# Optimization experiments

Hardware: AMD Instinct MI355X
Metric: run time of the kernel (lower is better)

Reference implementation:

```python
import jax, jax.numpy as jnp
import numpy as np

NT, NRV, NR = 100000, 200000, 300000  # tile / road_vertex / road node counts
E = 400000                             # edges per edge type
B, H, P, A = 64, 128, 64, 512          # graphs, hidden, player_state_dim, action_dim


def _gat(h_src, h_dst, src, dst, W, a_s, a_d, b, n_dst):
    # PyG GATConv, heads=1, shared lin for src/dst, no self loops (bipartite)
    hs = h_src @ W                      # [Ns, H]
    hd = h_dst @ W                      # [Nd, H]
    e = jax.nn.leaky_relu((hs @ a_s)[src] + (hd @ a_d)[dst], 0.2)  # [E]
    m = jax.ops.segment_max(e, dst, num_segments=n_dst)
    w = jnp.exp(e - m[dst])
    denom = jax.ops.segment_sum(w, dst, num_segments=n_dst)
    alpha = w / jnp.maximum(denom[dst], 1e-16)                      # segment softmax
    out = jax.ops.segment_sum(alpha[:, None] * hs[src], dst, num_segments=n_dst)
    return out + b


def _mean_pool(x, batch, nb):
    s = jax.ops.segment_sum(x, batch, num_segments=nb)
    c = jax.ops.segment_sum(jnp.ones((x.shape[0],), x.dtype), batch, num_segments=nb)
    return s / jnp.maximum(c, 1.0)[:, None]


def setup_inputs():
    ks = iter(jax.random.split(jax.random.key(0), 64))
    f32 = jnp.float32

    def lin(i, o):
        return (jax.random.normal(next(ks), (i, o), f32) / np.float32(np.sqrt(i)))

    d = {}
    d['x_tile'] = jax.random.normal(next(ks), (NT, 8), f32)
    d['x_rv'] = jax.random.normal(next(ks), (NRV, 13), f32)
    d['x_road'] = jax.random.normal(next(ks), (NR, 4), f32)
    d['x_player'] = jax.random.normal(next(ks), (B, P), f32)
    # node encoders
    d['enc_t_W'] = lin(8, H);  d['enc_t_b'] = jnp.zeros((H,), f32)
    d['enc_rv_W'] = lin(13, H); d['enc_rv_b'] = jnp.zeros((H,), f32)
    d['enc_r_W'] = lin(4, H);  d['enc_r_b'] = jnp.zeros((H,), f32)
    # six GAT convs
    for name in ['rv2t', 't2rv', 'r2rv', 'rv2r', 't2r', 'r2t']:
        d[name + '_W'] = lin(H, H)
        d[name + '_as'] = jax.random.normal(next(ks), (H,), f32) * 0.1
        d[name + '_ad'] = jax.random.normal(next(ks), (H,), f32) * 0.1
        d[name + '_b'] = jnp.zeros((H,), f32)
    # player MLP + output head (input: 3H pooled + H player)
    d['fc1_W'] = lin(P, H); d['fc1_b'] = jnp.zeros((H,), f32)
    d['fc2_W'] = lin(H, H); d['fc2_b'] = jnp.zeros((H,), f32)
    d['out_W'] = lin(4 * H, A); d['out_b'] = jnp.zeros((A,), f32)
    # edges (src bounded by source-type count, dst by dest-type count)
    ri = lambda n, hi: jax.random.randint(n, (E,), 0, hi, jnp.int32)
    d['e_rv2t_src'] = ri(next(ks), NRV); d['e_rv2t_dst'] = ri(next(ks), NT)
    d['e_t2rv_src'] = ri(next(ks), NT);  d['e_t2rv_dst'] = ri(next(ks), NRV)
    d['e_r2rv_src'] = ri(next(ks), NR);  d['e_r2rv_dst'] = ri(next(ks), NRV)
    d['e_rv2r_src'] = ri(next(ks), NRV); d['e_rv2r_dst'] = ri(next(ks), NR)
    d['e_t2r_src'] = ri(next(ks), NT);   d['e_t2r_dst'] = ri(next(ks), NR)
    d['e_r2t_src'] = ri(next(ks), NR);   d['e_r2t_dst'] = ri(next(ks), NT)
    # batch assignment per node type
    d['batch_tile'] = jnp.sort(jax.random.randint(next(ks), (NT,), 0, B, jnp.int32))
    d['batch_rv'] = jnp.sort(jax.random.randint(next(ks), (NRV,), 0, B, jnp.int32))
    d['batch_road'] = jnp.sort(jax.random.randint(next(ks), (NR,), 0, B, jnp.int32))
    return d


def reference(x_tile, x_rv, x_road, x_player,
              enc_t_W, enc_t_b, enc_rv_W, enc_rv_b, enc_r_W, enc_r_b,
              rv2t_W, rv2t_as, rv2t_ad, rv2t_b,
              t2rv_W, t2rv_as, t2rv_ad, t2rv_b,
              r2rv_W, r2rv_as, r2rv_ad, r2rv_b,
              rv2r_W, rv2r_as, rv2r_ad, rv2r_b,
              t2r_W, t2r_as, t2r_ad, t2r_b,
              r2t_W, r2t_as, r2t_ad, r2t_b,
              fc1_W, fc1_b, fc2_W, fc2_b, out_W, out_b,
              e_rv2t_src, e_rv2t_dst, e_t2rv_src, e_t2rv_dst,
              e_r2rv_src, e_r2rv_dst, e_rv2r_src, e_rv2r_dst,
              e_t2r_src, e_t2r_dst, e_r2t_src, e_r2t_dst,
              batch_tile, batch_rv, batch_road):
    # node encoders
    h_t = x_tile @ enc_t_W + enc_t_b
    h_rv = x_rv @ enc_rv_W + enc_rv_b
    h_r = x_road @ enc_r_W + enc_r_b
    # hetero GAT, aggr='sum' over edge types per destination node type
    o_t = (_gat(h_rv, h_t, e_rv2t_src, e_rv2t_dst, rv2t_W, rv2t_as, rv2t_ad, rv2t_b, NT)
           + _gat(h_r, h_t, e_r2t_src, e_r2t_dst, r2t_W, r2t_as, r2t_ad, r2t_b, NT))
    o_rv = (_gat(h_t, h_rv, e_t2rv_src, e_t2rv_dst, t2rv_W, t2rv_as, t2rv_ad, t2rv_b, NRV)
            + _gat(h_r, h_rv, e_r2rv_src, e_r2rv_dst, r2rv_W, r2rv_as, r2rv_ad, r2rv_b, NRV))
    o_r = (_gat(h_rv, h_r, e_rv2r_src, e_rv2r_dst, rv2r_W, rv2r_as, rv2r_ad, rv2r_b, NR)
           + _gat(h_t, h_r, e_t2r_src, e_t2r_dst, t2r_W, t2r_as, t2r_ad, t2r_b, NR))
    # global mean pool per node type, concat -> [B, 3H]
    x_all = jnp.concatenate([_mean_pool(o_t, batch_tile, B),
                             _mean_pool(o_rv, batch_rv, B),
                             _mean_pool(o_r, batch_road, B)], axis=1)
    # player branch
    p = jax.nn.relu(x_player @ fc1_W + fc1_b)
    p = jax.nn.relu(p @ fc2_W + fc2_b)
    x = jnp.concatenate([x_all, p], axis=1)  # [B, 4H]
    return x @ out_W + out_b                 # [B, A]
```

## Files before the change

kernel.cpp:

```cpp
#include <hip/hip_runtime.h>


constexpr int kNT = 100000, kNRV = 200000, kNR = 300000, kE = 400000;
constexpr int kEq   = kE / 4;
constexpr int kSLOT = 1088;
constexpr int kNBB  = 1024;

typedef _Float16 h2v __attribute__((ext_vector_type(2)));

constexpr long long OFF_C    = 0;
constexpr long long OFF_VS   = 13056;
constexpr long long OFF_VD   = 13176;
constexpr long long OFF_BD   = 13296;
constexpr long long OFF_PS   = 13512;
constexpr long long OFF_XCAT = 22216;
constexpr long long OFF_LS16 = 54984;
constexpr long long OFF_LD16 = 654984;
constexpr long long OFF_PB   = 54984;
constexpr long long OFF_W16  = 1254984;
constexpr long long OFF_DN   = 2454984;
constexpr long long OFF_XR   = 3654984;

__constant__ const int kLSB[6]  = {0, 200000, 300000, 600000, 800000, 900000};
__constant__ const int kDRB[6]  = {0, 100000, 300000, 500000, 800000, 1100000};
__constant__ const int kDLEN[6] = {100000, 200000, 200000, 300000, 300000, 100000};
__constant__ const int kDstT[6] = {0, 1, 1, 2, 2, 0};
__constant__ const int cSlotEt[8]  = {1, 2, 4, 5, 0, 0, 3, 3};
__constant__ const int cSlotLo[8]  = {0, 0, 0, 0, 0, 100000, 0, 100000};
__constant__ const int cSlotHi[8]  = {1 << 30, 1 << 30, 1 << 30, 1 << 30,
                                      100000, 200000, 100000, 200000};
__constant__ const int cSlotCnt[8] = {1, 1, 1, 1, 1, 0, 1, 0};

__device__ __forceinline__ int lowb(const int* a, int n, int v) {
  int lo = 0, hi = n;
  while (lo < hi) { int mid = (lo + hi) >> 1; if (a[mid] < v) lo = mid + 1; else hi = mid; }
  return lo;
}

__global__ __launch_bounds__(256) void precompute_kernel(
    const float* encW_t, const float* encb_t,
    const float* encW_rv, const float* encb_rv,
    const float* encW_r, const float* encb_r,
    const float* W0, const float* as0, const float* ad0,
    const float* W1, const float* as1, const float* ad1,
    const float* W2, const float* as2, const float* ad2,
    const float* W3, const float* as3, const float* ad3,
    const float* W4, const float* as4, const float* ad4,
    const float* W5, const float* as5, const float* ad5,
    const int* bt, const int* brv, const int* br,
    float* Cws, float* vsw, float* vdw, int* BD)
{
  int tid = threadIdx.x;
  if (blockIdx.x == 24) {
    if (tid < 3 * 65) {
      int tt = tid / 65, q = tid - tt * 65;
      const int* ba = (tt == 0) ? bt : (tt == 1 ? brv : br);
      int N = (tt == 0) ? kNT : (tt == 1 ? kNRV : kNR);
      BD[tt * 72 + q] = lowb(ba, N, q);
    }
    return;
  }
  const float* encW[3] = {encW_t, encW_rv, encW_r};
  const float* encb[3] = {encb_t, encb_rv, encb_r};
  const int    Ks[3]   = {8, 13, 4};
  const float* Wv[6]  = {W0, W1, W2, W3, W4, W5};
  const float* asv[6] = {as0, as1, as2, as3, as4, as5};
  const float* adv[6] = {ad0, ad1, ad2, ad3, ad4, ad5};
  const int srcT[6] = {1, 0, 2, 1, 0, 2};
  const int dstT[6] = {0, 1, 1, 2, 2, 0};

  int et = blockIdx.x >> 2;
  int jc = blockIdx.x & 3;
  int st = srcT[et], dt = dstT[et];
  const float* eW = encW[st];
  const float* eB = encb[st];
  int K = Ks[st];
  const float* W = Wv[et];

  float* Cslot = Cws + et * 2176;
  for (int idx = tid; idx < (K + 1) * 32; idx += 256) {
    int r = idx >> 5, jj = idx & 31;
    int j = jc * 32 + jj;
    const float* row = (r < K) ? (eW + r * 128) : eB;
    float acc = 0.f;
    for (int m = 0; m < 128; ++m) acc += row[m] * W[m * 128 + j];
    Cslot[(r < K) ? (r * 128 + j) : (2048 + j)] = acc;
  }

  if (jc == 0) {
    __shared__ float us[128], wvs[128];
    const float* a_s = asv[et];
    const float* a_d = adv[et];
    if (tid < 128) {
      float acc = 0.f;
      for (int j = 0; j < 128; ++j) acc += W[tid * 128 + j] * a_s[j];
      us[tid] = acc;
    } else {
      int m = tid - 128;
      float acc = 0.f;
      for (int j = 0; j < 128; ++j) acc += W[m * 128 + j] * a_d[j];
      wvs[m] = acc;
    }
    __syncthreads();
    if (tid <= K) {
      const float* row = (tid < K) ? (eW + tid * 128) : eB;
      float acc = 0.f;
      for (int m = 0; m < 128; ++m) acc += row[m] * us[m];
      vsw[et * 20 + (tid < K ? tid : 16)] = acc;
    }
    int KD = Ks[dt];
    if (tid >= 32 && tid <= 32 + KD) {
      int k = tid - 32;
      const float* row = (k < KD) ? (encW[dt] + k * 128) : encb[dt];
      float acc = 0.f;
      for (int m = 0; m < 128; ++m) acc += row[m] * wvs[m];
      vdw[et * 20 + (k < KD ? k : 16)] = acc;
    }
  }
}

template <int K, int RH>
__device__ __forceinline__ void prep_one(
    const float* __restrict__ xr,
    const float* __restrict__ vsA, const float* __restrict__ vsB,
    const float* __restrict__ vdA, const float* __restrict__ vdB,
    _Float16* lsA, _Float16* lsB, _Float16* ldA, _Float16* ldB,
    float* dnA, float* dnB, _Float16* xrec)
{
  float a0 = 0.f, a1 = 0.f, a2 = 0.f, a3 = 0.f;
#pragma unroll
  for (int k = 0; k < K; ++k) {
    float xv = xr[k];
    a0 += xv * vsA[k]; a1 += xv * vsB[k];
    a2 += xv * vdA[k]; a3 += xv * vdB[k];
    xrec[k] = (_Float16)xv;
  }
#pragma unroll
  for (int k = K; k < RH; ++k) xrec[k] = (_Float16)0.f;
  *lsA = (_Float16)(a0 + vsA[16]);
  *lsB = (_Float16)(a1 + vsB[16]);
  *ldA = (_Float16)(a2 + vdA[16]);
  *ldB = (_Float16)(a3 + vdB[16]);
  *dnA = 0.f;
  *dnB = 0.f;
}

__global__ __launch_bounds__(256) void prep_kernel(
    const float* __restrict__ x_t, const float* __restrict__ x_rv,
    const float* __restrict__ x_r,
    const float* __restrict__ vsw, const float* __restrict__ vdw,
    _Float16* __restrict__ LS16, _Float16* __restrict__ LD16,
    float* __restrict__ DN, _Float16* __restrict__ XR)
{
  int n = blockIdx.x * 256 + threadIdx.x;
  if (n >= kNT + kNRV + kNR) return;
  if (n < kNT) {
    prep_one<8, 8>(x_t + n * 8,
                   vsw + 1 * 20, vsw + 4 * 20, vdw + 0 * 20, vdw + 5 * 20,
                   LS16 + 200000 + n, LS16 + 800000 + n,
                   LD16 + 0 + n, LD16 + 1100000 + n,
                   DN + 0 + n, DN + 1100000 + n,
                   XR + (long long)n * 8);
  } else if (n < kNT + kNRV) {
    int m = n - kNT;
    prep_one<13, 16>(x_rv + m * 13,
                     vsw + 0 * 20, vsw + 3 * 20, vdw + 1 * 20, vdw + 2 * 20,
                     LS16 + 0 + m, LS16 + 600000 + m,
                     LD16 + 100000 + m, LD16 + 300000 + m,
                     DN + 100000 + m, DN + 300000 + m,
                     XR + 800000 + (long long)m * 16);
  } else {
    int m = n - kNT - kNRV;
    prep_one<4, 4>(x_r + m * 4,
                   vsw + 2 * 20, vsw + 5 * 20, vdw + 3 * 20, vdw + 4 * 20,
                   LS16 + 300000 + m, LS16 + 900000 + m,
                   LD16 + 500000 + m, LD16 + 800000 + m,
                   DN + 500000 + m, DN + 800000 + m,
                   XR + 4000000 + (long long)m * 4);
  }
}

__global__ __launch_bounds__(256) void passA_kernel(
    const int* s0, const int* s1, const int* s2,
    const int* s3, const int* s4, const int* s5,
    const int* d0, const int* d1, const int* d2,
    const int* d3, const int* d4, const int* d5,
    const _Float16* __restrict__ LS16, const _Float16* __restrict__ LD16,
    float* __restrict__ DN, _Float16* __restrict__ W16)
{
  int idx = blockIdx.x * 256 + threadIdx.x;
  if (idx >= 6 * kEq) return;
  int et = idx / kEq;
  int q = idx - et * kEq;
  const int* sp; const int* dp;
  switch (et) {
    case 0: sp = s0; dp = d0; break;
    case 1: sp = s1; dp = d1; break;
    case 2: sp = s2; dp = d2; break;
    case 3: sp = s3; dp = d3; break;
    case 4: sp = s4; dp = d4; break;
    default: sp = s5; dp = d5; break;
  }
  int lsb = kLSB[et], drb = kDRB[et];
  int4 ss = ((const int4*)sp)[q];
  int4 dd = ((const int4*)dp)[q];
  int sa[4] = {ss.x, ss.y, ss.z, ss.w};
  int da[4] = {dd.x, dd.y, dd.z, dd.w};
  union { float2 f; _Float16 h[4]; } WU;
  float wa[4];
#pragma unroll
  for (int i = 0; i < 4; ++i) {
    float t = (float)LS16[lsb + sa[i]] + (float)LD16[drb + da[i]];
    t = t > 0.f ? t : 0.2f * t;
    _Float16 h = (_Float16)__expf(t);
    WU.h[i] = h;
    wa[i] = (float)h;
  }
  ((float2*)(W16 + (long long)et * kE))[q] = WU.f;
#pragma unroll
  for (int i = 0; i < 4; ++i) unsafeAtomicAdd(&DN[drb + da[i]], wa[i]);
}

template <int RH>
__device__ __forceinline__ void loadX(const _Float16* __restrict__ xp, float* xv) {
  if constexpr (RH == 4) {
    union { uint2 u; _Float16 h[4]; } U;
    U.u = *(const uint2*)xp;
#pragma unroll
    for (int k = 0; k < RH; ++k) xv[k] = (float)U.h[k];
  } else if constexpr (RH == 8) {
    union { uint4 u; _Float16 h[8]; } U;
    U.u = *(const uint4*)xp;
#pragma unroll
    for (int k = 0; k < RH; ++k) xv[k] = (float)U.h[k];
  } else {
    union { uint4 u[2]; _Float16 h[16]; } U;
    U.u[0] = *(const uint4*)xp;
    U.u[1] = *(const uint4*)(xp + 8);
#pragma unroll
    for (int k = 0; k < RH; ++k) xv[k] = (float)U.h[k];
  }
}

template <int K, int RH>
__device__ __forceinline__ void passB_loop(
    const int* __restrict__ sp, const int* __restrict__ dp,
    const _Float16* __restrict__ Wet, const float* __restrict__ DN, int drb,
    const _Float16* __restrict__ XR, long long xrb,
    const int* __restrict__ bd, float* __restrict__ lp,
    int lo, int hi, int start, int stride)
{
  for (int q = start; q < kEq; q += stride) {
    int4 ss = ((const int4*)sp)[q];
    int4 dd = ((const int4*)dp)[q];
    union { float2 f; _Float16 h[4]; } WU;
    WU.f = ((const float2*)Wet)[q];
    int sa[4] = {ss.x, ss.y, ss.z, ss.w};
    int da[4] = {dd.x, dd.y, dd.z, dd.w};
#pragma unroll
    for (int i = 0; i < 4; ++i) {
      int s = sa[i], d = da[i];
      if (s >= lo && s < hi) {
        float dn = DN[drb + d];
        float alpha = (float)WU.h[i] / fmaxf(dn, 1e-16f);
        int b = 0;
#pragma unroll
        for (int stp = 32; stp >= 1; stp >>= 1) {
          int nb = b + stp;
          if (nb <= 63 && bd[nb] <= d) b = nb;
        }
        float xv[RH];
        loadX<RH>(XR + xrb + (long long)s * RH, xv);
#pragma unroll
        for (int k = 0; k < K; ++k) atomicAdd(lp + k * 64 + b, alpha * xv[k]);
      }
    }
  }
}

__global__ __launch_bounds__(256) void passB_kernel(
    const int* s0, const int* s1, const int* s2,
    const int* s3, const int* s4, const int* s5,
    const int* d0, const int* d1, const int* d2,
    const int* d3, const int* d4, const int* d5,
    const _Float16* __restrict__ W16, const float* __restrict__ DN,
    const _Float16* __restrict__ XR, const int* __restrict__ BDg,
    float* __restrict__ PB)
{
  __shared__ float lp[kSLOT];
  __shared__ int bd[65];
  int tid = threadIdx.x;
  for (int j = tid; j < kSLOT; j += 256) lp[j] = 0.f;
  int slot = blockIdx.x & 7;
  int blk = blockIdx.x >> 3;
  int et = cSlotEt[slot];
  if (tid < 65) bd[tid] = BDg[kDstT[et] * 72 + tid];
  __syncthreads();
  int lo = cSlotLo[slot], hi = cSlotHi[slot];
  int start = blk * 256 + tid;
  int stride = 128 * 256;
  int drb = kDRB[et];
  const _Float16* Wet = W16 + (long long)et * kE;
  switch (et) {
    case 0: passB_loop<13, 16>(s0, d0, Wet, DN, drb, XR, 800000,  bd, lp, lo, hi, start, stride); break;
    case 1: passB_loop< 8,  8>(s1, d1, Wet, DN, drb, XR, 0,       bd, lp, lo, hi, start, stride); break;
    case 2: passB_loop< 4,  4>(s2, d2, Wet, DN, drb, XR, 4000000, bd, lp, lo, hi, start, stride); break;
    case 3: passB_loop<13, 16>(s3, d3, Wet, DN, drb, XR, 800000,  bd, lp, lo, hi, start, stride); break;
    case 4: passB_loop< 8,  8>(s4, d4, Wet, DN, drb, XR, 0,       bd, lp, lo, hi, start, stride); break;
    default: passB_loop<4,  4>(s5, d5, Wet, DN, drb, XR, 4000000, bd, lp, lo, hi, start, stride); break;
  }
  if (cSlotCnt[slot]) {
    int dlen = kDLEN[et];
    for (int j = start; j < dlen; j += stride) {
      if (DN[drb + j] > 0.f) {
        int b = 0;
#pragma unroll
        for (int stp = 32; stp >= 1; stp >>= 1) {
          int nb = b + stp;
          if (nb <= 63 && bd[nb] <= j) b = nb;
        }
        atomicAdd(lp + 1024 + b, 1.f);
      }
    }
  }
  __syncthreads();
  float* dst = PB + (long long)blockIdx.x * kSLOT;
  for (int j = tid; j < kSLOT; j += 256) dst[j] = lp[j];
}

__global__ __launch_bounds__(256) void reduce1_kernel(
    const float* __restrict__ PB, float* __restrict__ PS)
{
  int slot = blockIdx.x / 5;
  int jb = blockIdx.x - slot * 5;
  int j = jb * 256 + threadIdx.x;
  if (j >= kSLOT) return;
  float s = 0.f;
#pragma unroll 8
  for (int blk = 0; blk < 128; ++blk)
    s += PB[(long long)(blk * 8 + slot) * kSLOT + j];
  PS[slot * kSLOT + j] = s;
}

__global__ __launch_bounds__(128) void finalize_kernel(
    const int* __restrict__ BDg,
    const float* __restrict__ xp,
    const float* __restrict__ fc1W, const float* __restrict__ fc1b,
    const float* __restrict__ fc2W, const float* __restrict__ fc2b,
    const float* __restrict__ b_rv2t, const float* __restrict__ b_r2t,
    const float* __restrict__ b_t2rv, const float* __restrict__ b_r2rv,
    const float* __restrict__ b_rv2r, const float* __restrict__ b_t2r,
    const float* __restrict__ Cws, const float* __restrict__ PS,
    float* __restrict__ xcat)
{
  int b = blockIdx.x, tid = threadIdx.x;
  __shared__ float xps[64];
  __shared__ float p1s[128];
  if (tid < 64) xps[tid] = xp[b * 64 + tid];
  __syncthreads();
  float a = fc1b[tid];
  for (int k = 0; k < 64; ++k) a += xps[k] * fc1W[k * 128 + tid];
  p1s[tid] = fmaxf(a, 0.f);
  __syncthreads();
  float a2 = fc2b[tid];
  for (int k = 0; k < 128; ++k) a2 += p1s[k] * fc2W[k * 128 + tid];
  xcat[b * 512 + 384 + tid] = fmaxf(a2, 0.f);

  const int etA[3] = {0, 1, 3}, etB[3] = {5, 2, 4};
  const int KAv[3] = {13, 8, 13}, KBv[3] = {4, 4, 8};
  const int slotA[6] = {4, 0, 1, 6, 2, 3};
  const int slotB[6] = {5, -1, -1, 7, -1, -1};
  for (int t3 = 0; t3 < 3; ++t3) {
    int eA = etA[t3], eB = etB[t3];
    const float* CA = Cws + eA * 2176;
    const float* CB = Cws + eB * 2176;
    int sA1 = slotA[eA], sA2 = slotB[eA];
    int sB1 = slotA[eB], sB2 = slotB[eB];
    const float* PA1 = PS + sA1 * kSLOT;
    const float* PA2 = (sA2 >= 0) ? (PS + sA2 * kSLOT) : nullptr;
    const float* PB1 = PS + sB1 * kSLOT;
    const float* PB2 = (sB2 >= 0) ? (PS + sB2 * kSLOT) : nullptr;
    float cA = PA1[1024 + b] + (PA2 ? PA2[1024 + b] : 0.f);
    float cB = PB1[1024 + b] + (PB2 ? PB2[1024 + b] : 0.f);
    float v = cA * CA[2048 + tid] + cB * CB[2048 + tid];
    for (int k = 0; k < KAv[t3]; ++k) {
      float pv = PA1[k * 64 + b] + (PA2 ? PA2[k * 64 + b] : 0.f);
      v += pv * CA[k * 128 + tid];
    }
    for (int k = 0; k < KBv[t3]; ++k) {
      float pv = PB1[k * 64 + b] + (PB2 ? PB2[k * 64 + b] : 0.f);
      v += pv * CB[k * 128 + tid];
    }
    int cnt = BDg[t3 * 72 + b + 1] - BDg[t3 * 72 + b];
    float cntf = (float)max(cnt, 1);
    const float* bb1 = (t3 == 0) ? b_rv2t : (t3 == 1 ? b_t2rv : b_rv2r);
    const float* bb2 = (t3 == 0) ? b_r2t  : (t3 == 1 ? b_r2rv : b_t2r);
    xcat[b * 512 + t3 * 128 + tid] = v / cntf + bb1[tid] + bb2[tid];
  }
}

__global__ __launch_bounds__(256) void out_kernel(
    const float* __restrict__ xcat, const float* __restrict__ outW,
    const float* __restrict__ outb, float* __restrict__ out)
{
  int g = blockIdx.x * 256 + threadIdx.x;
  int r = g >> 9, c = g & 511;
  const float* xr = xcat + r * 512;
  float acc = outb[c];
  for (int k = 0; k < 512; ++k) acc += xr[k] * outW[k * 512 + c];
  out[g] = acc;
}

extern "C" void kernel_launch(void* const* d_in, const int* in_sizes, int n_in,
                              void* d_out, int out_size, void* d_ws, size_t ws_size,
                              hipStream_t stream) {
  const float* x_tile   = (const float*)d_in[0];
  const float* x_rv     = (const float*)d_in[1];
  const float* x_road   = (const float*)d_in[2];
  const float* x_player = (const float*)d_in[3];
  const float* enc_t_W  = (const float*)d_in[4];
  const float* enc_t_b  = (const float*)d_in[5];
  const float* enc_rv_W = (const float*)d_in[6];
  const float* enc_rv_b = (const float*)d_in[7];
  const float* enc_r_W  = (const float*)d_in[8];
  const float* enc_r_b  = (const float*)d_in[9];
  const float* W[6]; const float* As[6]; const float* Ad[6]; const float* Bb[6];
  for (int et = 0; et < 6; ++et) {
    W[et]  = (const float*)d_in[10 + 4 * et];
    As[et] = (const float*)d_in[11 + 4 * et];
    Ad[et] = (const float*)d_in[12 + 4 * et];
    Bb[et] = (const float*)d_in[13 + 4 * et];
  }
  const float* fc1W = (const float*)d_in[34];
  const float* fc1b = (const float*)d_in[35];
  const float* fc2W = (const float*)d_in[36];
  const float* fc2b = (const float*)d_in[37];
  const float* outW = (const float*)d_in[38];
  const float* outb = (const float*)d_in[39];
  const int* esrc[6]; const int* edst[6];
  for (int et = 0; et < 6; ++et) {
    esrc[et] = (const int*)d_in[40 + 2 * et];
    edst[et] = (const int*)d_in[41 + 2 * et];
  }
  const int* batch_t  = (const int*)d_in[52];
  const int* batch_rv = (const int*)d_in[53];
  const int* batch_r  = (const int*)d_in[54];

  float* wsF = (float*)d_ws;
  float* Cws  = wsF + OFF_C;
  float* vsw  = wsF + OFF_VS;
  float* vdw  = wsF + OFF_VD;
  int*   BD   = (int*)(wsF + OFF_BD);
  float* PS   = wsF + OFF_PS;
  float* xcat = wsF + OFF_XCAT;
  _Float16* LS16 = (_Float16*)(wsF + OFF_LS16);
  _Float16* LD16 = (_Float16*)(wsF + OFF_LD16);
  float* PB   = wsF + OFF_PB;
  _Float16* W16 = (_Float16*)(wsF + OFF_W16);
  float* DN   = wsF + OFF_DN;
  _Float16* XR = (_Float16*)(wsF + OFF_XR);
  float* out  = (float*)d_out;

  precompute_kernel<<<25, 256, 0, stream>>>(
      enc_t_W, enc_t_b, enc_rv_W, enc_rv_b, enc_r_W, enc_r_b,
      W[0], As[0], Ad[0], W[1], As[1], Ad[1], W[2], As[2], Ad[2],
      W[3], As[3], Ad[3], W[4], As[4], Ad[4], W[5], As[5], Ad[5],
      batch_t, batch_rv, batch_r,
      Cws, vsw, vdw, BD);

  prep_kernel<<<(kNT + kNRV + kNR + 255) / 256, 256, 0, stream>>>(
      x_tile, x_rv, x_road, vsw, vdw, LS16, LD16, DN, XR);

  passA_kernel<<<(6 * kEq + 255) / 256, 256, 0, stream>>>(
      esrc[0], esrc[1], esrc[2], esrc[3], esrc[4], esrc[5],
      edst[0], edst[1], edst[2], edst[3], edst[4], edst[5],
      LS16, LD16, DN, W16);

  passB_kernel<<<kNBB, 256, 0, stream>>>(
      esrc[0], esrc[1], esrc[2], esrc[3], esrc[4], esrc[5],
      edst[0], edst[1], edst[2], edst[3], edst[4], edst[5],
      W16, DN, XR, BD, PB);

  reduce1_kernel<<<40, 256, 0, stream>>>(PB, PS);

  finalize_kernel<<<64, 128, 0, stream>>>(
      BD, x_player,
      fc1W, fc1b, fc2W, fc2b,
      Bb[0], Bb[5], Bb[1], Bb[2], Bb[3], Bb[4],
      Cws, PS, xcat);

  out_kernel<<<128, 256, 0, stream>>>(xcat, outW, outb, out);

  (void)in_sizes; (void)n_in; (void)out_size; (void)ws_size;
}
```

Before: 554.1 us.

## Pack reciprocal denominator with graph id into one word; retile passA/passB grids

```diff
diff --git a/kernel.cpp b/kernel.cpp
--- a/kernel.cpp
+++ b/kernel.cpp
@@ -4,9 +4,9 @@
 constexpr int kNT = 100000, kNRV = 200000, kNR = 300000, kE = 400000;
 constexpr int kEq   = kE / 4;
 constexpr int kSLOT = 1088;
-constexpr int kNBB  = 1024;
-
-typedef _Float16 h2v __attribute__((ext_vector_type(2)));
+constexpr int kNBB  = 1536;
+constexpr int kBPS  = 192;
+constexpr int kTOTD = 1200000;
 
 constexpr long long OFF_C    = 0;
 constexpr long long OFF_VS   = 13056;
@@ -16,15 +16,15 @@
 constexpr long long OFF_XCAT = 22216;
 constexpr long long OFF_LS16 = 54984;
 constexpr long long OFF_LD16 = 654984;
-constexpr long long OFF_PB   = 54984;
 constexpr long long OFF_W16  = 1254984;
 constexpr long long OFF_DN   = 2454984;
 constexpr long long OFF_XR   = 3654984;
+constexpr long long OFF_BID  = 6254984;
+constexpr long long OFF_PB   = 6554984;
 
 __constant__ const int kLSB[6]  = {0, 200000, 300000, 600000, 800000, 900000};
 __constant__ const int kDRB[6]  = {0, 100000, 300000, 500000, 800000, 1100000};
 __constant__ const int kDLEN[6] = {100000, 200000, 200000, 300000, 300000, 100000};
-__constant__ const int kDstT[6] = {0, 1, 1, 2, 2, 0};
 __constant__ const int cSlotEt[8]  = {1, 2, 4, 5, 0, 0, 3, 3};
 __constant__ const int cSlotLo[8]  = {0, 0, 0, 0, 0, 100000, 0, 100000};
 __constant__ const int cSlotHi[8]  = {1 << 30, 1 << 30, 1 << 30, 1 << 30,
@@ -121,11 +121,12 @@
 
 template <int K, int RH>
 __device__ __forceinline__ void prep_one(
-    const float* __restrict__ xr,
+    const float* __restrict__ xr, unsigned char b,
     const float* __restrict__ vsA, const float* __restrict__ vsB,
     const float* __restrict__ vdA, const float* __restrict__ vdB,
     _Float16* lsA, _Float16* lsB, _Float16* ldA, _Float16* ldB,
-    float* dnA, float* dnB, _Float16* xrec)
+    float* dnA, float* dnB, unsigned char* bidA, unsigned char* bidB,
+    _Float16* xrec)
 {
   float a0 = 0.f, a1 = 0.f, a2 = 0.f, a3 = 0.f;
 #pragma unroll
@@ -143,39 +144,47 @@
   *ldB = (_Float16)(a3 + vdB[16]);
   *dnA = 0.f;
   *dnB = 0.f;
+  *bidA = b;
+  *bidB = b;
 }
 
 __global__ __launch_bounds__(256) void prep_kernel(
     const float* __restrict__ x_t, const float* __restrict__ x_rv,
     const float* __restrict__ x_r,
+    const int* __restrict__ bt, const int* __restrict__ brv,
+    const int* __restrict__ br,
     const float* __restrict__ vsw, const float* __restrict__ vdw,
     _Float16* __restrict__ LS16, _Float16* __restrict__ LD16,
-    float* __restrict__ DN, _Float16* __restrict__ XR)
+    float* __restrict__ DN, unsigned char* __restrict__ BID,
+    _Float16* __restrict__ XR)
 {
   int n = blockIdx.x * 256 + threadIdx.x;
   if (n >= kNT + kNRV + kNR) return;
   if (n < kNT) {
-    prep_one<8, 8>(x_t + n * 8,
+    prep_one<8, 8>(x_t + n * 8, (unsigned char)bt[n],
                    vsw + 1 * 20, vsw + 4 * 20, vdw + 0 * 20, vdw + 5 * 20,
                    LS16 + 200000 + n, LS16 + 800000 + n,
                    LD16 + 0 + n, LD16 + 1100000 + n,
                    DN + 0 + n, DN + 1100000 + n,
+                   BID + 0 + n, BID + 1100000 + n,
                    XR + (long long)n * 8);
   } else if (n < kNT + kNRV) {
     int m = n - kNT;
-    prep_one<13, 16>(x_rv + m * 13,
+    prep_one<13, 16>(x_rv + m * 13, (unsigned char)brv[m],
                      vsw + 0 * 20, vsw + 3 * 20, vdw + 1 * 20, vdw + 2 * 20,
                      LS16 + 0 + m, LS16 + 600000 + m,
                      LD16 + 100000 + m, LD16 + 300000 + m,
                      DN + 100000 + m, DN + 300000 + m,
+                     BID + 100000 + m, BID + 300000 + m,
                      XR + 800000 + (long long)m * 16);
   } else {
     int m = n - kNT - kNRV;
-    prep_one<4, 4>(x_r + m * 4,
+    prep_one<4, 4>(x_r + m * 4, (unsigned char)br[m],
                    vsw + 2 * 20, vsw + 5 * 20, vdw + 3 * 20, vdw + 4 * 20,
                    LS16 + 300000 + m, LS16 + 900000 + m,
                    LD16 + 500000 + m, LD16 + 800000 + m,
                    DN + 500000 + m, DN + 800000 + m,
+                   BID + 500000 + m, BID + 800000 + m,
                    XR + 4000000 + (long long)m * 4);
   }
 }
@@ -188,37 +197,53 @@
     const _Float16* __restrict__ LS16, const _Float16* __restrict__ LD16,
     float* __restrict__ DN, _Float16* __restrict__ W16)
 {
-  int idx = blockIdx.x * 256 + threadIdx.x;
-  if (idx >= 6 * kEq) return;
-  int et = idx / kEq;
-  int q = idx - et * kEq;
-  const int* sp; const int* dp;
-  switch (et) {
-    case 0: sp = s0; dp = d0; break;
-    case 1: sp = s1; dp = d1; break;
-    case 2: sp = s2; dp = d2; break;
-    case 3: sp = s3; dp = d3; break;
-    case 4: sp = s4; dp = d4; break;
-    default: sp = s5; dp = d5; break;
-  }
-  int lsb = kLSB[et], drb = kDRB[et];
-  int4 ss = ((const int4*)sp)[q];
-  int4 dd = ((const int4*)dp)[q];
-  int sa[4] = {ss.x, ss.y, ss.z, ss.w};
-  int da[4] = {dd.x, dd.y, dd.z, dd.w};
-  union { float2 f; _Float16 h[4]; } WU;
-  float wa[4];
-#pragma unroll
-  for (int i = 0; i < 4; ++i) {
-    float t = (float)LS16[lsb + sa[i]] + (float)LD16[drb + da[i]];
-    t = t > 0.f ? t : 0.2f * t;
-    _Float16 h = (_Float16)__expf(t);
-    WU.h[i] = h;
-    wa[i] = (float)h;
-  }
-  ((float2*)(W16 + (long long)et * kE))[q] = WU.f;
-#pragma unroll
-  for (int i = 0; i < 4; ++i) unsafeAtomicAdd(&DN[drb + da[i]], wa[i]);
+  int slot = blockIdx.x & 7;
+  int blk = blockIdx.x >> 3;
+  for (int i = blk * 256 + (int)threadIdx.x; i < 75000; i += kBPS * 256) {
+    int gq = slot * 75000 + i;
+    int et = gq / 100000;
+    int q = gq - et * 100000;
+    const int* sp; const int* dp;
+    switch (et) {
+      case 0: sp = s0; dp = d0; break;
+      case 1: sp = s1; dp = d1; break;
+      case 2: sp = s2; dp = d2; break;
+      case 3: sp = s3; dp = d3; break;
+      case 4: sp = s4; dp = d4; break;
+      default: sp = s5; dp = d5; break;
+    }
+    int lsb = kLSB[et], drb = kDRB[et];
+    int4 ss = ((const int4*)sp)[q];
+    int4 dd = ((const int4*)dp)[q];
+    int sa[4] = {ss.x, ss.y, ss.z, ss.w};
+    int da[4] = {dd.x, dd.y, dd.z, dd.w};
+    union { float2 f; _Float16 h[4]; } WU;
+    float wa[4];
+#pragma unroll
+    for (int j = 0; j < 4; ++j) {
+      float t = (float)LS16[lsb + sa[j]] + (float)LD16[drb + da[j]];
+      t = t > 0.f ? t : 0.2f * t;
+      _Float16 h = (_Float16)__expf(t);
+      WU.h[j] = h;
+      wa[j] = (float)h;
+    }
+    ((float2*)(W16 + (long long)et * kE))[q] = WU.f;
+#pragma unroll
+    for (int j = 0; j < 4; ++j) unsafeAtomicAdd(&DN[drb + da[j]], wa[j]);
+  }
+}
+
+__global__ __launch_bounds__(256) void pack_kernel(
+    const float* __restrict__ DN, const unsigned char* __restrict__ BID,
+    unsigned* __restrict__ DNu)
+{
+  int j = blockIdx.x * 256 + threadIdx.x;
+  if (j >= kTOTD) return;
+  float dn = DN[j];
+  unsigned u = 0u;
+  if (dn > 0.f)
+    u = (__float_as_uint(1.f / dn) & ~63u) | (unsigned)BID[j];
+  DNu[j] = u;
 }
 
 template <int RH>
@@ -245,10 +270,9 @@
 template <int K, int RH>
 __device__ __forceinline__ void passB_loop(
     const int* __restrict__ sp, const int* __restrict__ dp,
-    const _Float16* __restrict__ Wet, const float* __restrict__ DN, int drb,
+    const _Float16* __restrict__ Wet, const unsigned* __restrict__ DNu, int drb,
     const _Float16* __restrict__ XR, long long xrb,
-    const int* __restrict__ bd, float* __restrict__ lp,
-    int lo, int hi, int start, int stride)
+    float* __restrict__ lp, int lo, int hi, int start, int stride)
 {
   for (int q = start; q < kEq; q += stride) {
     int4 ss = ((const int4*)sp)[q];
@@ -261,14 +285,10 @@
     for (int i = 0; i < 4; ++i) {
       int s = sa[i], d = da[i];
       if (s >= lo && s < hi) {
-        float dn = DN[drb + d];
-        float alpha = (float)WU.h[i] / fmaxf(dn, 1e-16f);
-        int b = 0;
-#pragma unroll
-        for (int stp = 32; stp >= 1; stp >>= 1) {
-          int nb = b + stp;
-          if (nb <= 63 && bd[nb] <= d) b = nb;
-        }
+        unsigned u = DNu[drb + d];
+        int b = (int)(u & 63u);
+        float rinv = __uint_as_float(u & ~63u);
+        float alpha = (float)WU.h[i] * rinv;
         float xv[RH];
         loadX<RH>(XR + xrb + (long long)s * RH, xv);
 #pragma unroll
@@ -283,44 +303,34 @@
     const int* s3, const int* s4, const int* s5,
     const int* d0, const int* d1, const int* d2,
     const int* d3, const int* d4, const int* d5,
-    const _Float16* __restrict__ W16, const float* __restrict__ DN,
-    const _Float16* __restrict__ XR, const int* __restrict__ BDg,
-    float* __restrict__ PB)
+    const _Float16* __restrict__ W16, const unsigned* __restrict__ DNu,
+    const _Float16* __restrict__ XR, float* __restrict__ PB)
 {
   __shared__ float lp[kSLOT];
-  __shared__ int bd[65];
   int tid = threadIdx.x;
   for (int j = tid; j < kSLOT; j += 256) lp[j] = 0.f;
+  __syncthreads();
   int slot = blockIdx.x & 7;
   int blk = blockIdx.x >> 3;
   int et = cSlotEt[slot];
-  if (tid < 65) bd[tid] = BDg[kDstT[et] * 72 + tid];
-  __syncthreads();
   int lo = cSlotLo[slot], hi = cSlotHi[slot];
   int start = blk * 256 + tid;
-  int stride = 128 * 256;
+  int stride = kBPS * 256;
   int drb = kDRB[et];
   const _Float16* Wet = W16 + (long long)et * kE;
   switch (et) {
-    case 0: passB_loop<13, 16>(s0, d0, Wet, DN, drb, XR, 800000,  bd, lp, lo, hi, start, stride); break;
-    case 1: passB_loop< 8,  8>(s1, d1, Wet, DN, drb, XR, 0,       bd, lp, lo, hi, start, stride); break;
-    case 2: passB_loop< 4,  4>(s2, d2, Wet, DN, drb, XR, 4000000, bd, lp, lo, hi, start, stride); break;
-    case 3: passB_loop<13, 16>(s3, d3, Wet, DN, drb, XR, 800000,  bd, lp, lo, hi, start, stride); break;
-    case 4: passB_loop< 8,  8>(s4, d4, Wet, DN, drb, XR, 0,       bd, lp, lo, hi, start, stride); break;
-    default: passB_loop<4,  4>(s5, d5, Wet, DN, drb, XR, 4000000, bd, lp, lo, hi, start, stride); break;
+    case 0: passB_loop<13, 16>(s0, d0, Wet, DNu, drb, XR, 800000,  lp, lo, hi, start, stride); break;
+    case 1: passB_loop< 8,  8>(s1, d1, Wet, DNu, drb, XR, 0,       lp, lo, hi, start, stride); break;
+    case 2: passB_loop< 4,  4>(s2, d2, Wet, DNu, drb, XR, 4000000, lp, lo, hi, start, stride); break;
+    case 3: passB_loop<13, 16>(s3, d3, Wet, DNu, drb, XR, 800000,  lp, lo, hi, start, stride); break;
+    case 4: passB_loop< 8,  8>(s4, d4, Wet, DNu, drb, XR, 0,       lp, lo, hi, start, stride); break;
+    default: passB_loop<4,  4>(s5, d5, Wet, DNu, drb, XR, 4000000, lp, lo, hi, start, stride); break;
   }
   if (cSlotCnt[slot]) {
     int dlen = kDLEN[et];
     for (int j = start; j < dlen; j += stride) {
-      if (DN[drb + j] > 0.f) {
-        int b = 0;
-#pragma unroll
-        for (int stp = 32; stp >= 1; stp >>= 1) {
-          int nb = b + stp;
-          if (nb <= 63 && bd[nb] <= j) b = nb;
-        }
-        atomicAdd(lp + 1024 + b, 1.f);
-      }
+      unsigned u = DNu[drb + j];
+      if (u >> 6) atomicAdd(lp + 1024 + (int)(u & 63u), 1.f);
     }
   }
   __syncthreads();
@@ -337,7 +347,7 @@
   if (j >= kSLOT) return;
   float s = 0.f;
 #pragma unroll 8
-  for (int blk = 0; blk < 128; ++blk)
+  for (int blk = 0; blk < kBPS; ++blk)
     s += PB[(long long)(blk * 8 + slot) * kSLOT + j];
   PS[slot * kSLOT + j] = s;
 }
@@ -455,10 +465,12 @@
   float* xcat = wsF + OFF_XCAT;
   _Float16* LS16 = (_Float16*)(wsF + OFF_LS16);
   _Float16* LD16 = (_Float16*)(wsF + OFF_LD16);
-  float* PB   = wsF + OFF_PB;
   _Float16* W16 = (_Float16*)(wsF + OFF_W16);
   float* DN   = wsF + OFF_DN;
+  unsigned* DNu = (unsigned*)(wsF + OFF_DN);
   _Float16* XR = (_Float16*)(wsF + OFF_XR);
+  unsigned char* BID = (unsigned char*)(wsF + OFF_BID);
+  float* PB   = wsF + OFF_PB;
   float* out  = (float*)d_out;
 
   precompute_kernel<<<25, 256, 0, stream>>>(
@@ -469,17 +481,20 @@
       Cws, vsw, vdw, BD);
 
   prep_kernel<<<(kNT + kNRV + kNR + 255) / 256, 256, 0, stream>>>(
-      x_tile, x_rv, x_road, vsw, vdw, LS16, LD16, DN, XR);
-
-  passA_kernel<<<(6 * kEq + 255) / 256, 256, 0, stream>>>(
+      x_tile, x_rv, x_road, batch_t, batch_rv, batch_r, vsw, vdw,
+      LS16, LD16, DN, BID, XR);
+
+  passA_kernel<<<kNBB, 256, 0, stream>>>(
       esrc[0], esrc[1], esrc[2], esrc[3], esrc[4], esrc[5],
       edst[0], edst[1], edst[2], edst[3], edst[4], edst[5],
       LS16, LD16, DN, W16);
 
+  pack_kernel<<<(kTOTD + 255) / 256, 256, 0, stream>>>(DN, BID, DNu);
+
   passB_kernel<<<kNBB, 256, 0, stream>>>(
       esrc[0], esrc[1], esrc[2], esrc[3], esrc[4], esrc[5],
       edst[0], edst[1], edst[2], edst[3], edst[4], edst[5],
-      W16, DN, XR, BD, PB);
+      W16, DNu, XR, PB);
 
   reduce1_kernel<<<40, 256, 0, stream>>>(PB, PS);
 
```

Result: no change. 556.1 us (+0.4%).
